# Kernel optimization log

Measured on AMD Instinct MI355X. Metric: run time of the kernel, lower is better.

Reference implementation:

```python
import jax, jax.numpy as jnp
import numpy as np

B, S, D_MODEL, H = 4, 2048, 1024, 16
DEPTH = D_MODEL // H


def setup_inputs() -> dict:
    key = jax.random.key(0)
    ks = jax.random.split(key, 12)
    std = 1.0 / np.sqrt(D_MODEL)
    inp = {
        "q": jax.random.normal(ks[0], (B, S, D_MODEL), jnp.float32),
        "k": jax.random.normal(ks[1], (B, S, D_MODEL), jnp.float32),
        "v": jax.random.normal(ks[2], (B, S, D_MODEL), jnp.float32),
        # causal mask: 1.0 where attention is disallowed (j > i)
        "mask": jnp.triu(jnp.ones((S, S), jnp.float32), k=1)[None, None, :, :],
        "wq_w": jax.random.normal(ks[3], (D_MODEL, D_MODEL), jnp.float32) * std,
        "wq_b": jnp.zeros((D_MODEL,), jnp.float32),
        "wk_w": jax.random.normal(ks[4], (D_MODEL, D_MODEL), jnp.float32) * std,
        "wk_b": jnp.zeros((D_MODEL,), jnp.float32),
        "wv_w": jax.random.normal(ks[5], (D_MODEL, D_MODEL), jnp.float32) * std,
        "wv_b": jnp.zeros((D_MODEL,), jnp.float32),
        "wo_w": jax.random.normal(ks[6], (D_MODEL, D_MODEL), jnp.float32) * std,
        "wo_b": jnp.zeros((D_MODEL,), jnp.float32),
    }
    return inp


def _split_heads(x):
    # [B, S, D_MODEL] -> [B, H, S, DEPTH]
    b, s, _ = x.shape
    return x.reshape(b, s, H, DEPTH).transpose(0, 2, 1, 3)


def reference(q, k, v, mask, wq_w, wq_b, wk_w, wk_b, wv_w, wv_b, wo_w, wo_b):
    # torch.nn.Linear: y = x @ W.T + b
    qh = _split_heads(q @ wq_w.T + wq_b)
    kh = _split_heads(k @ wk_w.T + wk_b)
    vh = _split_heads(v @ wv_w.T + wv_b)
    scale = 1.0 / jnp.sqrt(jnp.asarray(DEPTH, jnp.float32))
    logits = jnp.einsum("bhqd,bhkd->bhqk", qh, kh) * scale
    logits = logits + mask * (-1e9)
    attn = jax.nn.softmax(logits, axis=-1)  # [B, H, Sq, Sk]
    ctx = jnp.einsum("bhqk,bhkd->bhqd", attn, vh)
    concat = ctx.transpose(0, 2, 1, 3).reshape(q.shape[0], -1, D_MODEL)
    out = concat @ wo_w.T + wo_b
    return (out, attn)
```

## Files before the change

kernel.cpp:

```cpp
#include <hip/hip_runtime.h>
#include <hip/hip_bf16.h>

typedef __hip_bfloat16 bf16;
typedef unsigned short u16;
typedef _Float16 f16;
typedef u16 u16x8 __attribute__((ext_vector_type(8)));
typedef f16 f16x8 __attribute__((ext_vector_type(8)));
typedef float f32x4 __attribute__((ext_vector_type(4)));

#define B_ 4
#define S_ 2048
#define DM_ 1024
#define H_ 16
#define DEPTH_ 64
#define M_ (B_ * S_)

#define OUT_ELEMS ((size_t)M_ * DM_)
#define QKV_ELEMS ((size_t)B_ * H_ * S_ * DEPTH_)

__global__ void detect_kernel(const unsigned* __restrict__ mask, int* __restrict__ flag) {
  *flag = (mask[0] != 0u) ? 1 : 0;
}

__device__ __forceinline__ float loadf(const void* p, size_t i, int bf) {
  return bf ? __bfloat162float(((const bf16*)p)[i]) : ((const float*)p)[i];
}
__device__ __forceinline__ void storef(void* p, size_t i, float v, int bf) {
  if (bf)
    ((bf16*)p)[i] = __float2bfloat16(v);
  else
    ((float*)p)[i] = v;
}

__device__ __forceinline__ u16 f32_to_f16_bits(float f) {
  return __builtin_bit_cast(u16, (f16)f);
}
__device__ __forceinline__ u16 f32_to_bf16_bits(float f) {
  bf16 b = __float2bfloat16(f);
  return __builtin_bit_cast(u16, b);
}
__device__ __forceinline__ float bf_bits_to_f32(u16 h) {
  unsigned u = (unsigned)h << 16;
  return __builtin_bit_cast(float, u);
}

__device__ __forceinline__ void gload_lds16(const void* g, void* l) {
  __builtin_amdgcn_global_load_lds(
      (__attribute__((address_space(1))) void*)(uintptr_t)g,
      (__attribute__((address_space(3))) void*)(uintptr_t)l, 16, 0, 0);
}

__global__ __launch_bounds__(256) void cvt_f16_kernel(const void* __restrict__ src,
                                                      u16* __restrict__ dst, int n8,
                                                      const int* __restrict__ flagp) {
  int i = blockIdx.x * 256 + threadIdx.x;
  if (i >= n8) return;
  const int bf = *flagp;
  u16x8 o;
  if (bf) {
    u16x8 s = ((const u16x8*)src)[i];
#pragma unroll
    for (int t = 0; t < 8; ++t) o[t] = f32_to_f16_bits(bf_bits_to_f32(s[t]));
  } else {
    const float4* sp = (const float4*)src;
    float4 x = sp[2 * i], y = sp[2 * i + 1];
    o[0] = f32_to_f16_bits(x.x);
    o[1] = f32_to_f16_bits(x.y);
    o[2] = f32_to_f16_bits(x.z);
    o[3] = f32_to_f16_bits(x.w);
    o[4] = f32_to_f16_bits(y.x);
    o[5] = f32_to_f16_bits(y.y);
    o[6] = f32_to_f16_bits(y.z);
    o[7] = f32_to_f16_bits(y.w);
  }
  ((u16x8*)dst)[i] = o;
}

__global__ __launch_bounds__(256) void cvt_bias_kernel(const void* b0, const void* b1,
                                                       const void* b2, const void* b3,
                                                       float* __restrict__ dst,
                                                       const int* __restrict__ flagp) {
  int i = blockIdx.x * 256 + threadIdx.x;
  const int bf = *flagp;
  const void* s = (i < 1024) ? b0 : (i < 2048) ? b1 : (i < 3072) ? b2 : b3;
  dst[i] = loadf(s, i & 1023, bf);
}

template <bool OUT_RAW>
__global__ __launch_bounds__(256) void gemm_f16(const u16* __restrict__ A,
                                                const u16* __restrict__ W,
                                                const float* __restrict__ biasf,
                                                void* __restrict__ out,
                                                const int* __restrict__ flagp,
                                                int M, int N, int K) {
  __shared__ alignas(16) u16 As[128 * 32];
  __shared__ alignas(16) u16 Ws[128 * 32];
  const int tid = threadIdx.x;
  const int wave = tid >> 6, lane = tid & 63;
  const int wr = wave >> 1, wc = wave & 1;
  const int fr = lane & 15, fq = lane >> 4;
  const int tm = blockIdx.x * 128, tn = blockIdx.y * 128;
  f32x4 acc[4][4] = {};

  for (int k0 = 0; k0 < K; k0 += 32) {
#pragma unroll
    for (int t = 0; t < 2; ++t) {
      int li = wave * 128 + t * 64 + lane;
      int r = li >> 2, s2 = li & 3;
      gload_lds16(A + (size_t)(tm + r) * K + k0 + s2 * 8,
                  (char*)As + (size_t)(wave * 2 + t) * 1024);
      gload_lds16(W + (size_t)(tn + r) * K + k0 + s2 * 8,
                  (char*)Ws + (size_t)(wave * 2 + t) * 1024);
    }
    __syncthreads();
    f16x8 a[4], b[4];
#pragma unroll
    for (int i = 0; i < 4; ++i)
      a[i] = *(const f16x8*)&As[(wr * 64 + i * 16 + fr) * 32 + fq * 8];
#pragma unroll
    for (int j = 0; j < 4; ++j)
      b[j] = *(const f16x8*)&Ws[(wc * 64 + j * 16 + fr) * 32 + fq * 8];
#pragma unroll
    for (int i = 0; i < 4; ++i)
#pragma unroll
      for (int j = 0; j < 4; ++j)
        acc[i][j] = __builtin_amdgcn_mfma_f32_16x16x32_f16(a[i], b[j], acc[i][j], 0, 0, 0);
    __syncthreads();
  }

  const int bfflag = *flagp;
  float bv[4];
#pragma unroll
  for (int j = 0; j < 4; ++j) bv[j] = biasf[tn + wc * 64 + j * 16 + fr];
#pragma unroll
  for (int i = 0; i < 4; ++i) {
#pragma unroll
    for (int j = 0; j < 4; ++j) {
#pragma unroll
      for (int r = 0; r < 4; ++r) {
        int m = tm + wr * 64 + i * 16 + fq * 4 + r;
        int n = tn + wc * 64 + j * 16 + fr;
        float v = acc[i][j][r] + bv[j];
        if (OUT_RAW) {
          storef(out, (size_t)m * N + n, v, bfflag);
        } else {
          int b_ = m >> 11, s_ = m & (S_ - 1);
          int h_ = n >> 6, d_ = n & 63;
          size_t idx = (((size_t)(b_ * H_ + h_)) * S_ + s_) * DEPTH_ + d_;
          ((u16*)out)[idx] = f32_to_f16_bits(v);
        }
      }
    }
  }
}

__device__ __forceinline__ void stage_tile64(const u16* g, u16* lds, int wave, int lane) {
#pragma unroll
  for (int t = 0; t < 2; ++t) {
    int si = wave * 128 + t * 64 + lane;
    int row = si >> 3;
    int cs = (si & 7) ^ (row & 7);
    gload_lds16(g + (size_t)row * 64 + cs * 8, (char*)lds + (size_t)(wave * 128 + t * 64) * 16);
  }
}
__device__ __forceinline__ f16x8 lds_frag(const u16* lds, int row, int slot) {
  return *(const f16x8*)&lds[(size_t)(row * 8 + (slot ^ (row & 7))) * 8];
}

__global__ __launch_bounds__(256) void attn_mfma(const u16* __restrict__ qh,
                                                 const u16* __restrict__ kh,
                                                 const u16* __restrict__ vh,
                                                 void* __restrict__ d_out,
                                                 u16* __restrict__ ctx,
                                                 const int* __restrict__ flagp) {
  const int bf = *flagp;
  const int rt = blockIdx.x;
  const int bh = blockIdx.y;
  const int b = bh >> 4, h = bh & (H_ - 1);
  const int i0 = rt * 64;
  const float scale = 0.125f;
  __shared__ alignas(16) u16 Qs[64 * 64];
  __shared__ alignas(16) u16 Ks[64 * 64];
  __shared__ alignas(16) u16 Vt[64 * 72];
  __shared__ alignas(16) u16 Ps[64 * 72];
  const int tid = threadIdx.x;
  const int wave = tid >> 6, lane = tid & 63;
  const int fr = lane & 15, fq = lane >> 4;
  const u16* qb = qh + (size_t)bh * S_ * DEPTH_;
  const u16* kb = kh + (size_t)bh * S_ * DEPTH_;
  const u16* vb = vh + (size_t)bh * S_ * DEPTH_;
  char* attnp = (char*)d_out + OUT_ELEMS * (bf ? 2 : 4);

  const int qrow = wave * 16 + fr;
  const int grow = i0 + qrow;

  stage_tile64(qb + (size_t)i0 * 64, Qs, wave, lane);
  __syncthreads();
  f16x8 qf[2];
#pragma unroll
  for (int ks = 0; ks < 2; ++ks) qf[ks] = lds_frag(Qs, qrow, ks * 4 + fq);

  float m_r = -1e30f, l_r = 0.f;

  for (int kt = 0; kt <= rt; ++kt) {
    __syncthreads();
    stage_tile64(kb + (size_t)kt * 64 * 64, Ks, wave, lane);
    __syncthreads();
    f32x4 sa[4] = {};
#pragma unroll
    for (int mi = 0; mi < 4; ++mi)
#pragma unroll
      for (int ks = 0; ks < 2; ++ks) {
        f16x8 af = lds_frag(Ks, mi * 16 + fr, ks * 4 + fq);
        sa[mi] = __builtin_amdgcn_mfma_f32_16x16x32_f16(af, qf[ks], sa[mi], 0, 0, 0);
      }
    const bool diag = (kt == rt);
    float sc[4][4];
    float tmax = -1e30f;
#pragma unroll
    for (int mi = 0; mi < 4; ++mi)
#pragma unroll
      for (int r = 0; r < 4; ++r) {
        int col = kt * 64 + mi * 16 + fq * 4 + r;
        float s = sa[mi][r] * scale;
        if (diag && col > grow) s = -1e30f;
        sc[mi][r] = s;
        tmax = fmaxf(tmax, s);
      }
    tmax = fmaxf(tmax, __shfl_xor(tmax, 16));
    tmax = fmaxf(tmax, __shfl_xor(tmax, 32));
    float mn = fmaxf(m_r, tmax);
    float sum = 0.f;
#pragma unroll
    for (int mi = 0; mi < 4; ++mi)
#pragma unroll
      for (int r = 0; r < 4; ++r) sum += __expf(sc[mi][r] - mn);
    sum += __shfl_xor(sum, 16);
    sum += __shfl_xor(sum, 32);
    l_r = l_r * __expf(m_r - mn) + sum;
    m_r = mn;
  }
  const float m_fin = m_r;
  const float linv = 1.0f / l_r;

  f32x4 ctxa[4] = {};
  for (int kt = 0; kt <= rt; ++kt) {
    __syncthreads();
    stage_tile64(kb + (size_t)kt * 64 * 64, Ks, wave, lane);
    {
      int k = tid >> 2, d0 = (tid & 3) * 16;
      const u16* vrow = vb + (size_t)(kt * 64 + k) * 64 + d0;
      u16x8 v0 = *(const u16x8*)vrow;
      u16x8 v1 = *(const u16x8*)(vrow + 8);
#pragma unroll
      for (int t = 0; t < 8; ++t) {
        Vt[(d0 + t) * 72 + k] = v0[t];
        Vt[(d0 + 8 + t) * 72 + k] = v1[t];
      }
    }
    __syncthreads();
    f32x4 sa[4] = {};
#pragma unroll
    for (int mi = 0; mi < 4; ++mi)
#pragma unroll
      for (int ks = 0; ks < 2; ++ks) {
        f16x8 af = lds_frag(Ks, mi * 16 + fr, ks * 4 + fq);
        sa[mi] = __builtin_amdgcn_mfma_f32_16x16x32_f16(af, qf[ks], sa[mi], 0, 0, 0);
      }
    const bool diag = (kt == rt);
    float p[4][4];
#pragma unroll
    for (int mi = 0; mi < 4; ++mi)
#pragma unroll
      for (int r = 0; r < 4; ++r) {
        int col = kt * 64 + mi * 16 + fq * 4 + r;
        float s = sa[mi][r] * scale;
        p[mi][r] = (diag && col > grow) ? 0.f : __expf(s - m_fin) * linv;
      }
    size_t rbase = ((size_t)bh * S_ + grow) * S_ + (size_t)kt * 64;
    if (bf) {
#pragma unroll
      for (int mi = 0; mi < 4; ++mi) {
        ushort4 o;
        o.x = f32_to_bf16_bits(p[mi][0]);
        o.y = f32_to_bf16_bits(p[mi][1]);
        o.z = f32_to_bf16_bits(p[mi][2]);
        o.w = f32_to_bf16_bits(p[mi][3]);
        *(ushort4*)((u16*)attnp + rbase + mi * 16 + fq * 4) = o;
      }
    } else {
#pragma unroll
      for (int mi = 0; mi < 4; ++mi) {
        float4 o = {p[mi][0], p[mi][1], p[mi][2], p[mi][3]};
        *(float4*)((float*)attnp + rbase + mi * 16 + fq * 4) = o;
      }
    }
#pragma unroll
    for (int mi = 0; mi < 4; ++mi)
#pragma unroll
      for (int j = 0; j < 2; ++j) {
        unsigned pk = (unsigned)f32_to_f16_bits(p[mi][2 * j]) |
                      ((unsigned)f32_to_f16_bits(p[mi][2 * j + 1]) << 16);
        *(unsigned*)&Ps[(size_t)qrow * 72 + mi * 16 + fq * 4 + 2 * j] = pk;
      }
    f16x8 pa[2];
#pragma unroll
    for (int ks = 0; ks < 2; ++ks)
      pa[ks] = *(const f16x8*)&Ps[(size_t)qrow * 72 + ks * 32 + fq * 8];
#pragma unroll
    for (int nj = 0; nj < 4; ++nj)
#pragma unroll
      for (int ks = 0; ks < 2; ++ks) {
        f16x8 vf = *(const f16x8*)&Vt[(size_t)(nj * 16 + fr) * 72 + ks * 32 + fq * 8];
        ctxa[nj] = __builtin_amdgcn_mfma_f32_16x16x32_f16(pa[ks], vf, ctxa[nj], 0, 0, 0);
      }
  }

  {
    int r = tid >> 2, c = (tid & 3) * 16;
    for (int kt = rt + 1; kt < S_ / 64; ++kt) {
      size_t abase = ((size_t)bh * S_ + i0 + r) * S_ + (size_t)kt * 64 + c;
      if (bf) {
        u16x8 z = {};
        *(u16x8*)((u16*)attnp + abase) = z;
        *(u16x8*)((u16*)attnp + abase + 8) = z;
      } else {
        float4 z = {};
        float* ap = (float*)attnp + abase;
        *(float4*)ap = z;
        *(float4*)(ap + 4) = z;
        *(float4*)(ap + 8) = z;
        *(float4*)(ap + 12) = z;
      }
    }
  }

  __syncthreads();
#pragma unroll
  for (int nj = 0; nj < 4; ++nj)
#pragma unroll
    for (int r = 0; r < 4; ++r)
      Ps[(size_t)(wave * 16 + fq * 4 + r) * 72 + nj * 16 + fr] = f32_to_f16_bits(ctxa[nj][r]);
  __syncthreads();
  {
    int lr = tid >> 2, c0 = (tid & 3) * 16;
    u16x8 o0 = *(const u16x8*)&Ps[(size_t)lr * 72 + c0];
    u16x8 o1 = *(const u16x8*)&Ps[(size_t)lr * 72 + c0 + 8];
    u16* cbp = ctx + ((size_t)b * S_ + i0 + lr) * DM_ + h * DEPTH_ + c0;
    *(u16x8*)cbp = o0;
    *(u16x8*)(cbp + 8) = o1;
  }
}

extern "C" void kernel_launch(void* const* d_in, const int* in_sizes, int n_in,
                              void* d_out, int out_size, void* d_ws, size_t ws_size,
                              hipStream_t stream) {
  const void* q = d_in[0];
  const void* k = d_in[1];
  const void* v = d_in[2];
  const unsigned* mask_u = (const unsigned*)d_in[3];
  const void* wq_w = d_in[4];
  const void* wq_b = d_in[5];
  const void* wk_w = d_in[6];
  const void* wk_b = d_in[7];
  const void* wv_w = d_in[8];
  const void* wv_b = d_in[9];
  const void* wo_w = d_in[10];
  const void* wo_b = d_in[11];

  u16* ws = (u16*)d_ws;
  u16* qh = ws;
  u16* kh = ws + QKV_ELEMS;
  u16* vh = ws + 2 * QKV_ELEMS;
  u16* cbuf = ws + 3 * QKV_ELEMS;
  u16* wbuf = ws + 4 * QKV_ELEMS;
  float* biasf = (float*)(wbuf + 4 * (size_t)DM_ * DM_);
  int* flagp = (int*)(biasf + 4 * 1024);

  detect_kernel<<<1, 1, 0, stream>>>(mask_u, flagp);
  cvt_bias_kernel<<<16, 256, 0, stream>>>(wq_b, wk_b, wv_b, wo_b, biasf, flagp);

  const int W8 = DM_ * DM_ / 8;
  cvt_f16_kernel<<<W8 / 256, 256, 0, stream>>>(wq_w, wbuf + 0 * (size_t)DM_ * DM_, W8, flagp);
  cvt_f16_kernel<<<W8 / 256, 256, 0, stream>>>(wk_w, wbuf + 1 * (size_t)DM_ * DM_, W8, flagp);
  cvt_f16_kernel<<<W8 / 256, 256, 0, stream>>>(wv_w, wbuf + 2 * (size_t)DM_ * DM_, W8, flagp);
  cvt_f16_kernel<<<W8 / 256, 256, 0, stream>>>(wo_w, wbuf + 3 * (size_t)DM_ * DM_, W8, flagp);

  const int Q8 = (int)(OUT_ELEMS / 8);
  dim3 gg(M_ / 128, DM_ / 128);

  cvt_f16_kernel<<<Q8 / 256, 256, 0, stream>>>(q, cbuf, Q8, flagp);
  gemm_f16<false><<<gg, 256, 0, stream>>>(cbuf, wbuf + 0 * (size_t)DM_ * DM_, biasf + 0, qh,
                                          flagp, M_, DM_, DM_);
  cvt_f16_kernel<<<Q8 / 256, 256, 0, stream>>>(k, cbuf, Q8, flagp);
  gemm_f16<false><<<gg, 256, 0, stream>>>(cbuf, wbuf + 1 * (size_t)DM_ * DM_, biasf + 1024, kh,
                                          flagp, M_, DM_, DM_);
  cvt_f16_kernel<<<Q8 / 256, 256, 0, stream>>>(v, cbuf, Q8, flagp);
  gemm_f16<false><<<gg, 256, 0, stream>>>(cbuf, wbuf + 2 * (size_t)DM_ * DM_, biasf + 2048, vh,
                                          flagp, M_, DM_, DM_);

  attn_mfma<<<dim3(S_ / 64, B_ * H_), 256, 0, stream>>>(qh, kh, vh, d_out, cbuf, flagp);

  gemm_f16<true><<<gg, 256, 0, stream>>>(cbuf, wbuf + 3 * (size_t)DM_ * DM_, biasf + 3072, d_out,
                                         flagp, M_, DM_, DM_);
}
```

Measured before the change: 1.510 ms.

## Fuse input conversion into batched QKV GEMM, merge weight casts, raise MFMA priority

Replaces the separate per-tensor fp16 conversion passes and three QKV GEMM launches with one 3D-grid GEMM that reads the raw fp32/bf16 activations, converts them in registers, and writes them to LDS. The four weight conversions become a single launch. s_setprio is raised around MFMA loops in the attention kernel. The aim is to remove the intermediate round-trip of converted activations and the launch overhead. The A operand is now loaded synchronously rather than via async global_load_lds, which may expose load latency inside the GEMM loop.

```diff
diff --git a/kernel.cpp b/kernel.cpp
--- a/kernel.cpp
+++ b/kernel.cpp
@@ -44,36 +44,42 @@
   return __builtin_bit_cast(float, u);
 }
 
+__device__ __forceinline__ f16x8 cvt8_from_f32(const float* p) {
+  float4 x = *(const float4*)p, y = *(const float4*)(p + 4);
+  f16x8 o;
+  o[0] = (f16)x.x; o[1] = (f16)x.y; o[2] = (f16)x.z; o[3] = (f16)x.w;
+  o[4] = (f16)y.x; o[5] = (f16)y.y; o[6] = (f16)y.z; o[7] = (f16)y.w;
+  return o;
+}
+__device__ __forceinline__ f16x8 cvt8_from_bf16(const u16* p) {
+  u16x8 s = *(const u16x8*)p;
+  f16x8 o;
+#pragma unroll
+  for (int t = 0; t < 8; ++t) o[t] = (f16)bf_bits_to_f32(s[t]);
+  return o;
+}
+
 __device__ __forceinline__ void gload_lds16(const void* g, void* l) {
   __builtin_amdgcn_global_load_lds(
       (__attribute__((address_space(1))) void*)(uintptr_t)g,
       (__attribute__((address_space(3))) void*)(uintptr_t)l, 16, 0, 0);
 }
 
-__global__ __launch_bounds__(256) void cvt_f16_kernel(const void* __restrict__ src,
-                                                      u16* __restrict__ dst, int n8,
-                                                      const int* __restrict__ flagp) {
+__global__ __launch_bounds__(256) void cvt_w_kernel(const void* w0, const void* w1,
+                                                    const void* w2, const void* w3,
+                                                    u16* __restrict__ dst,
+                                                    const int* __restrict__ flagp) {
   int i = blockIdx.x * 256 + threadIdx.x;
-  if (i >= n8) return;
   const int bf = *flagp;
-  u16x8 o;
-  if (bf) {
-    u16x8 s = ((const u16x8*)src)[i];
-#pragma unroll
-    for (int t = 0; t < 8; ++t) o[t] = f32_to_f16_bits(bf_bits_to_f32(s[t]));
-  } else {
-    const float4* sp = (const float4*)src;
-    float4 x = sp[2 * i], y = sp[2 * i + 1];
-    o[0] = f32_to_f16_bits(x.x);
-    o[1] = f32_to_f16_bits(x.y);
-    o[2] = f32_to_f16_bits(x.z);
-    o[3] = f32_to_f16_bits(x.w);
-    o[4] = f32_to_f16_bits(y.x);
-    o[5] = f32_to_f16_bits(y.y);
-    o[6] = f32_to_f16_bits(y.z);
-    o[7] = f32_to_f16_bits(y.w);
-  }
-  ((u16x8*)dst)[i] = o;
+  int sel = i >> 17;
+  const void* s = (sel == 0) ? w0 : (sel == 1) ? w1 : (sel == 2) ? w2 : w3;
+  int j = i & 131071;
+  f16x8 o;
+  if (bf)
+    o = cvt8_from_bf16((const u16*)s + (size_t)j * 8);
+  else
+    o = cvt8_from_f32((const float*)s + (size_t)j * 8);
+  ((f16x8*)dst)[i] = o;
 }
 
 __global__ __launch_bounds__(256) void cvt_bias_kernel(const void* b0, const void* b1,
@@ -86,13 +92,95 @@
   dst[i] = loadf(s, i & 1023, bf);
 }
 
-template <bool OUT_RAW>
-__global__ __launch_bounds__(256) void gemm_f16(const u16* __restrict__ A,
-                                                const u16* __restrict__ W,
+__global__ __launch_bounds__(256) void qkv_gemm(const void* __restrict__ qraw,
+                                                const void* __restrict__ kraw,
+                                                const void* __restrict__ vraw,
+                                                const u16* __restrict__ wbuf,
                                                 const float* __restrict__ biasf,
-                                                void* __restrict__ out,
-                                                const int* __restrict__ flagp,
-                                                int M, int N, int K) {
+                                                u16* __restrict__ qkvh,
+                                                const int* __restrict__ flagp) {
+  const int z = blockIdx.z;
+  const void* A = (z == 0) ? qraw : (z == 1) ? kraw : vraw;
+  const u16* W = wbuf + (size_t)z * DM_ * DM_;
+  const float* bias = biasf + z * 1024;
+  u16* out = qkvh + (size_t)z * QKV_ELEMS;
+  const int bf = *flagp;
+  const int K = DM_;
+
+  __shared__ alignas(16) u16 As[128 * 32];
+  __shared__ alignas(16) u16 Ws[128 * 32];
+  const int tid = threadIdx.x;
+  const int wave = tid >> 6, lane = tid & 63;
+  const int wr = wave >> 1, wc = wave & 1;
+  const int fr = lane & 15, fq = lane >> 4;
+  const int tm = blockIdx.x * 128, tn = blockIdx.y * 128;
+  const int arow = tid >> 1;
+  const int acol = (tid & 1) * 16;
+  f32x4 acc[4][4] = {};
+
+  for (int k0 = 0; k0 < K; k0 += 32) {
+    f16x8 a0, a1;
+    if (bf) {
+      const u16* ap = (const u16*)A + (size_t)(tm + arow) * K + k0 + acol;
+      a0 = cvt8_from_bf16(ap);
+      a1 = cvt8_from_bf16(ap + 8);
+    } else {
+      const float* ap = (const float*)A + (size_t)(tm + arow) * K + k0 + acol;
+      a0 = cvt8_from_f32(ap);
+      a1 = cvt8_from_f32(ap + 8);
+    }
+    *(f16x8*)&As[(size_t)arow * 32 + acol] = a0;
+    *(f16x8*)&As[(size_t)arow * 32 + acol + 8] = a1;
+#pragma unroll
+    for (int t = 0; t < 2; ++t) {
+      int li = wave * 128 + t * 64 + lane;
+      int r = li >> 2, s2 = li & 3;
+      gload_lds16(W + (size_t)(tn + r) * K + k0 + s2 * 8,
+                  (char*)Ws + (size_t)(wave * 2 + t) * 1024);
+    }
+    __syncthreads();
+    f16x8 a[4], b[4];
+#pragma unroll
+    for (int i = 0; i < 4; ++i)
+      a[i] = *(const f16x8*)&As[(wr * 64 + i * 16 + fr) * 32 + fq * 8];
+#pragma unroll
+    for (int j = 0; j < 4; ++j)
+      b[j] = *(const f16x8*)&Ws[(wc * 64 + j * 16 + fr) * 32 + fq * 8];
+#pragma unroll
+    for (int i = 0; i < 4; ++i)
+#pragma unroll
+      for (int j = 0; j < 4; ++j)
+        acc[i][j] = __builtin_amdgcn_mfma_f32_16x16x32_f16(a[i], b[j], acc[i][j], 0, 0, 0);
+    __syncthreads();
+  }
+
+  float bv[4];
+#pragma unroll
+  for (int j = 0; j < 4; ++j) bv[j] = bias[tn + wc * 64 + j * 16 + fr];
+#pragma unroll
+  for (int i = 0; i < 4; ++i) {
+#pragma unroll
+    for (int j = 0; j < 4; ++j) {
+#pragma unroll
+      for (int r = 0; r < 4; ++r) {
+        int m = tm + wr * 64 + i * 16 + fq * 4 + r;
+        int n = tn + wc * 64 + j * 16 + fr;
+        float v = acc[i][j][r] + bv[j];
+        int b_ = m >> 11, s_ = m & (S_ - 1);
+        int h_ = n >> 6, d_ = n & 63;
+        size_t idx = (((size_t)(b_ * H_ + h_)) * S_ + s_) * DEPTH_ + d_;
+        out[idx] = f32_to_f16_bits(v);
+      }
+    }
+  }
+}
+
+__global__ __launch_bounds__(256) void wo_gemm(const u16* __restrict__ A,
+                                               const u16* __restrict__ W,
+                                               const float* __restrict__ biasf,
+                                               void* __restrict__ out,
+                                               const int* __restrict__ flagp,
+                                               int M, int N, int K) {
   __shared__ alignas(16) u16 As[128 * 32];
   __shared__ alignas(16) u16 Ws[128 * 32];
   const int tid = threadIdx.x;
@@ -140,15 +228,7 @@
       for (int r = 0; r < 4; ++r) {
         int m = tm + wr * 64 + i * 16 + fq * 4 + r;
         int n = tn + wc * 64 + j * 16 + fr;
-        float v = acc[i][j][r] + bv[j];
-        if (OUT_RAW) {
-          storef(out, (size_t)m * N + n, v, bfflag);
-        } else {
-          int b_ = m >> 11, s_ = m & (S_ - 1);
-          int h_ = n >> 6, d_ = n & 63;
-          size_t idx = (((size_t)(b_ * H_ + h_)) * S_ + s_) * DEPTH_ + d_;
-          ((u16*)out)[idx] = f32_to_f16_bits(v);
-        }
+        storef(out, (size_t)m * N + n, acc[i][j][r] + bv[j], bfflag);
       }
     }
   }
@@ -207,6 +287,7 @@
     stage_tile64(kb + (size_t)kt * 64 * 64, Ks, wave, lane);
     __syncthreads();
     f32x4 sa[4] = {};
+    __builtin_amdgcn_s_setprio(1);
 #pragma unroll
     for (int mi = 0; mi < 4; ++mi)
 #pragma unroll
@@ -214,6 +295,7 @@
         f16x8 af = lds_frag(Ks, mi * 16 + fr, ks * 4 + fq);
         sa[mi] = __builtin_amdgcn_mfma_f32_16x16x32_f16(af, qf[ks], sa[mi], 0, 0, 0);
       }
+    __builtin_amdgcn_s_setprio(0);
     const bool diag = (kt == rt);
     float sc[4][4];
     float tmax = -1e30f;
@@ -260,6 +342,7 @@
     }
     __syncthreads();
     f32x4 sa[4] = {};
+    __builtin_amdgcn_s_setprio(1);
 #pragma unroll
     for (int mi = 0; mi < 4; ++mi)
 #pragma unroll
@@ -267,6 +350,7 @@
         f16x8 af = lds_frag(Ks, mi * 16 + fr, ks * 4 + fq);
         sa[mi] = __builtin_amdgcn_mfma_f32_16x16x32_f16(af, qf[ks], sa[mi], 0, 0, 0);
       }
+    __builtin_amdgcn_s_setprio(0);
     const bool diag = (kt == rt);
     float p[4][4];
 #pragma unroll
@@ -307,6 +391,7 @@
 #pragma unroll
     for (int ks = 0; ks < 2; ++ks)
       pa[ks] = *(const f16x8*)&Ps[(size_t)qrow * 72 + ks * 32 + fq * 8];
+    __builtin_amdgcn_s_setprio(1);
 #pragma unroll
     for (int nj = 0; nj < 4; ++nj)
 #pragma unroll
@@ -314,6 +399,7 @@
         f16x8 vf = *(const f16x8*)&Vt[(size_t)(nj * 16 + fr) * 72 + ks * 32 + fq * 8];
         ctxa[nj] = __builtin_amdgcn_mfma_f32_16x16x32_f16(pa[ks], vf, ctxa[nj], 0, 0, 0);
       }
+    __builtin_amdgcn_s_setprio(0);
   }
 
   {
@@ -369,9 +455,7 @@
   const void* wo_b = d_in[11];
 
   u16* ws = (u16*)d_ws;
-  u16* qh = ws;
-  u16* kh = ws + QKV_ELEMS;
-  u16* vh = ws + 2 * QKV_ELEMS;
+  u16* qkvh = ws;
   u16* cbuf = ws + 3 * QKV_ELEMS;
   u16* wbuf = ws + 4 * QKV_ELEMS;
   float* biasf = (float*)(wbuf + 4 * (size_t)DM_ * DM_);
@@ -379,28 +463,14 @@
 
   detect_kernel<<<1, 1, 0, stream>>>(mask_u, flagp);
   cvt_bias_kernel<<<16, 256, 0, stream>>>(wq_b, wk_b, wv_b, wo_b, biasf, flagp);
-
-  const int W8 = DM_ * DM_ / 8;
-  cvt_f16_kernel<<<W8 / 256, 256, 0, stream>>>(wq_w, wbuf + 0 * (size_t)DM_ * DM_, W8, flagp);
-  cvt_f16_kernel<<<W8 / 256, 256, 0, stream>>>(wk_w, wbuf + 1 * (size_t)DM_ * DM_, W8, flagp);
-  cvt_f16_kernel<<<W8 / 256, 256, 0, stream>>>(wv_w, wbuf + 2 * (size_t)DM_ * DM_, W8, flagp);
-  cvt_f16_kernel<<<W8 / 256, 256, 0, stream>>>(wo_w, wbuf + 3 * (size_t)DM_ * DM_, W8, flagp);
-
-  const int Q8 = (int)(OUT_ELEMS / 8);
-  dim3 gg(M_ / 128, DM_ / 128);
-
-  cvt_f16_kernel<<<Q8 / 256, 256, 0, stream>>>(q, cbuf, Q8, flagp);
-  gemm_f16<false><<<gg, 256, 0, stream>>>(cbuf, wbuf + 0 * (size_t)DM_ * DM_, biasf + 0, qh,
-                                          flagp, M_, DM_, DM_);
-  cvt_f16_kernel<<<Q8 / 256, 256, 0, stream>>>(k, cbuf, Q8, flagp);
-  gemm_f16<false><<<gg, 256, 0, stream>>>(cbuf, wbuf + 1 * (size_t)DM_ * DM_, biasf + 1024, kh,
-                                          flagp, M_, DM_, DM_);
-  cvt_f16_kernel<<<Q8 / 256, 256, 0, stream>>>(v, cbuf, Q8, flagp);
-  gemm_f16<false><<<gg, 256, 0, stream>>>(cbuf, wbuf + 2 * (size_t)DM_ * DM_, biasf + 2048, vh,
-                                          flagp, M_, DM_, DM_);
-
-  attn_mfma<<<dim3(S_ / 64, B_ * H_), 256, 0, stream>>>(qh, kh, vh, d_out, cbuf, flagp);
-
-  gemm_f16<true><<<gg, 256, 0, stream>>>(cbuf, wbuf + 3 * (size_t)DM_ * DM_, biasf + 3072, d_out,
-                                         flagp, M_, DM_, DM_);
-}
+  cvt_w_kernel<<<2048, 256, 0, stream>>>(wq_w, wk_w, wv_w, wo_w, wbuf, flagp);
+
+  dim3 gq(M_ / 128, DM_ / 128, 3);
+  qkv_gemm<<<gq, 256, 0, stream>>>(q, k, v, wbuf, biasf, qkvh, flagp);
+
+  attn_mfma<<<dim3(S_ / 64, B_ * H_), 256, 0, stream>>>(qkvh, qkvh + QKV_ELEMS,
+                                                        qkvh + 2 * QKV_ELEMS, d_out, cbuf, flagp);
+
+  wo_gemm<<<dim3(M_ / 128, DM_ / 128), 256, 0, stream>>>(
+      cbuf, wbuf + 3 * (size_t)DM_ * DM_, biasf + 3072, d_out, flagp, M_, DM_, DM_);
+}
```

Result: no change. 1.489 ms (-1.4%).
